# Kernel optimization log

Measured on AMD Instinct MI355X. Metric: run time of the kernel, lower is better.

## Reference

```python
import jax, jax.numpy as jnp
import numpy as np

NUM_NODES = 6144
INPUT_DIM = 128
OUTPUT_DIM = 128
NUM_HEADS = 4
HEAD_DIM = OUTPUT_DIM // NUM_HEADS
NEG_INF = -9e15  # mask constant used by the original module


def setup_inputs() -> dict:
    key = jax.random.key(0)
    k_x, k_adj, k_W, k_a = jax.random.split(key, 4)
    x = jax.random.normal(k_x, (NUM_NODES, INPUT_DIM), dtype=jnp.float32)
    adj = jax.random.randint(k_adj, (NUM_NODES, NUM_NODES), 0, 2, dtype=jnp.int32)
    # kaiming-uniform-ish init scale
    W = jax.random.uniform(k_W, (NUM_HEADS, INPUT_DIM, HEAD_DIM), dtype=jnp.float32,
                           minval=-1.0, maxval=1.0) * np.sqrt(6.0 / INPUT_DIM)
    a = jax.random.uniform(k_a, (NUM_HEADS, 2 * HEAD_DIM, 1), dtype=jnp.float32,
                           minval=-1.0, maxval=1.0) * np.sqrt(6.0 / (2 * HEAD_DIM))
    return {"x": x, "adj": adj, "W": W, "a": a}


def reference(x, adj, W, a):
    # x: [N, Din], adj: [N, N] int, W: [H, Din, d], a: [H, 2d, 1]
    H, Din, d = W.shape
    N = x.shape[0]
    h = jnp.einsum('ni,hid->hnd', x, W)               # [H, N, d] per-head projections
    a_dst = a[:, :d, 0]                                # applied to h_j (column / source of message)
    a_src = a[:, d:, 0]                                # applied to h_i (row / destination)
    s_dst = jnp.einsum('hnd,hd->hn', h, a_dst)         # [H, N]
    s_src = jnp.einsum('hnd,hd->hn', h, a_src)         # [H, N]
    # energy[h, i, j] = leaky_relu(a1 . h_j + a2 . h_i), same as concat-attention
    energy = jax.nn.leaky_relu(s_src[:, :, None] + s_dst[:, None, :], negative_slope=0.2)
    energy = jnp.where(adj[None] > 0, energy, NEG_INF)  # [H, N, N]
    attention = jax.nn.softmax(energy, axis=-1)
    h_prime = jnp.einsum('hij,hjd->hid', attention, h)  # [H, N, d]
    # faithful to torch h_prime.view(num_nodes, -1) on a contiguous [H,N,d] tensor
    return jnp.reshape(h_prime, (N, H * d))
```

## Files before the change

### kernel.cpp

```cpp
#include <hip/hip_runtime.h>
#include <stdint.h>

#define N_NODES 6144
#define LOG2E 1.44269504088896f

typedef float f32x4 __attribute__((ext_vector_type(4)));
typedef float f32x2 __attribute__((ext_vector_type(2)));
typedef short short8 __attribute__((ext_vector_type(8)));
typedef unsigned int uint32;
typedef unsigned long long uint64;

extern "C" __device__ float __ocml_native_exp2_f32(float);

__device__ __forceinline__ unsigned int pack2bf(float a, float b) {
  unsigned int ua = __float_as_uint(a) + 0x8000u;
  unsigned int ub = __float_as_uint(b) + 0x8000u;
  return __builtin_amdgcn_perm(ub, ua, 0x07060302u);
}

__device__ __forceinline__ uint32 bitmask32(uint32 bits, int j) {
#if __has_builtin(__builtin_amdgcn_sbfe)
  return (uint32)__builtin_amdgcn_sbfe((int)bits, (uint32)j, 1u);
#else
  return (uint32)(((int)(bits << (31 - j))) >> 31);
#endif
}

__global__ __launch_bounds__(256) void k0_pack(const int* __restrict__ adj,
                                               uint64* __restrict__ mask64) {
  int t = threadIdx.x;
  int wid = t >> 6, lane = t & 63;
  int row = blockIdx.x * 4 + wid;
  const int* ar = adj + (size_t)row * N_NODES + lane;
  uint64* mr = mask64 + (size_t)row * 96;
  #pragma unroll 8
  for (int c = 0; c < 96; ++c) {
    int v = ar[c << 6];
    uint64 b = __ballot(v != 0);
    if (lane == (c & 63)) mr[c] = b;
  }
}

__global__ __launch_bounds__(256) void k1_feat(const float* __restrict__ x,
                                               const float* __restrict__ W,
                                               const float* __restrict__ a,
                                               unsigned short* __restrict__ hfF,
                                               float* __restrict__ s_src2,
                                               float* __restrict__ s_dst2) {
  __shared__ float xl[64][132];
  __shared__ float Wl[64][128];
  int t = threadIdx.x;
  int n0 = blockIdx.x * 64;
  for (int u = t; u < 2048; u += 256) {
    int row = u >> 5, c4 = (u & 31) << 2;
    *(float4*)&xl[row][c4] = *(const float4*)(x + (size_t)(n0 + row) * 128 + c4);
  }
  int cg = t & 31, c0 = cg << 2;
  int ng = t >> 5, nb = ng << 3;
  float acc[8][4] = {};
  for (int ic = 0; ic < 2; ++ic) {
    __syncthreads();
    for (int u = t; u < 2048; u += 256) {
      int ii = u >> 5, c4 = (u & 31) << 2;
      int hh = c4 >> 5, d0 = c4 & 31;
      *(float4*)&Wl[ii][c4] = *(const float4*)(W + hh * 4096 + (ic * 64 + ii) * 32 + d0);
    }
    __syncthreads();
    #pragma unroll 4
    for (int ii = 0; ii < 64; ++ii) {
      float4 wv = *(float4*)&Wl[ii][c0];
      int i = ic * 64 + ii;
      #pragma unroll
      for (int r = 0; r < 8; ++r) {
        float xv = xl[nb + r][i];
        acc[r][0] += xv * wv.x; acc[r][1] += xv * wv.y;
        acc[r][2] += xv * wv.z; acc[r][3] += xv * wv.w;
      }
    }
  }
  __syncthreads();
  unsigned short* tb = (unsigned short*)&xl[0][0];
  float* pb = &Wl[0][0];
  int hh = c0 >> 5, d0 = c0 & 31;
  float4 adv = *(const float4*)(a + hh * 64 + d0);
  float4 asv = *(const float4*)(a + hh * 64 + 32 + d0);
  #pragma unroll
  for (int cc = 0; cc < 4; ++cc) {
    unsigned int* dst = (unsigned int*)(tb + (c0 + cc) * 66 + nb);
    #pragma unroll
    for (int p = 0; p < 4; ++p)
      dst[p] = pack2bf(acc[2 * p][cc], acc[2 * p + 1][cc]);
  }
  #pragma unroll
  for (int r = 0; r < 8; ++r) {
    float pd = acc[r][0] * adv.x + acc[r][1] * adv.y + acc[r][2] * adv.z + acc[r][3] * adv.w;
    float ps = acc[r][0] * asv.x + acc[r][1] * asv.y + acc[r][2] * asv.z + acc[r][3] * asv.w;
    pb[(nb + r) * 33 + cg] = pd;
    pb[2112 + (nb + r) * 33 + cg] = ps;
  }
  __syncthreads();
  {
    #pragma unroll
    for (int p = 0; p < 4; ++p) {
      int chunk = (p << 2) + (t >> 6);
      int lane = t & 63, mm = lane & 15, qq = lane >> 4;
      int h2 = chunk >> 2, kbl = (chunk >> 1) & 1, ff = chunk & 1;
      const unsigned int* s32 = (const unsigned int*)(
          tb + (h2 * 32 + ff * 16 + mm) * 66 + kbl * 32 + (qq << 3));
      int4 v;
      v.x = s32[0]; v.y = s32[1]; v.z = s32[2]; v.w = s32[3];
      int kbg = (n0 >> 5) + kbl;
      *(int4*)(hfF + (size_t)(((h2 * 192 + kbg) * 2 + ff) * 64 + lane) * 8) = v;
    }
  }
  for (int task = t; task < 512; task += 256) {
    int n = task & 63, hz = task >> 6;
    int h = hz & 3, sdx = hz >> 2;
    const float* src = pb + sdx * 2112 + n * 33 + h * 8;
    float s = src[0] + src[1] + src[2] + src[3] + src[4] + src[5] + src[6] + src[7];
    float* out = sdx ? s_src2 : s_dst2;
    out[h * N_NODES + n0 + n] = s * LOG2E;
  }
}

__device__ __forceinline__ void gat_tile(float ss, uint32 bits8,
                                         const f32x2 (&dv)[4], short8 b0, short8 b1,
                                         short8 ones, f32x4& a0, f32x4& a1, f32x4& az) {
  union { uint32 u4[4]; short8 v; } afr;
  f32x2 ss2;
  ss2[0] = ss; ss2[1] = ss;
  #pragma unroll
  for (int p = 0; p < 4; ++p) {
    f32x2 e = ss2 + dv[p];
    f32x2 e5 = e * 0.2f;
    float lrl = fmaxf(e[0], e5[0]);
    float lrh = fmaxf(e[1], e5[1]);
    float exl = __ocml_native_exp2_f32(lrl);
    float exh = __ocml_native_exp2_f32(lrh);
    uint32 wl = __float_as_uint(exl) & bitmask32(bits8, 2 * p);
    uint32 wh = __float_as_uint(exh) & bitmask32(bits8, 2 * p + 1);
    uint32 pk;
    asm("v_cvt_pk_bf16_f32 %0, %1, %2"
        : "=v"(pk)
        : "v"(__uint_as_float(wl)), "v"(__uint_as_float(wh)));
    afr.u4[p] = pk;
  }
  a0 = __builtin_amdgcn_mfma_f32_16x16x32_bf16(afr.v, b0, a0, 0, 0, 0);
  a1 = __builtin_amdgcn_mfma_f32_16x16x32_bf16(afr.v, b1, a1, 0, 0, 0);
  az = __builtin_amdgcn_mfma_f32_16x16x32_bf16(afr.v, ones, az, 0, 0, 0);
}

__device__ __forceinline__ void step2(uint32 w0, uint32 w1,
                                      int sh, const float* sdp, int koff,
                                      int4 B0i, int4 B1i, short8 ones,
                                      float ss0, float ss1,
                                      f32x4& a00, f32x4& a01, f32x4& a10, f32x4& a11,
                                      f32x4& az0, f32x4& az1) {
  union { f32x4 q[2]; f32x2 d[4]; } du;
  du.q[0] = *(const f32x4*)(sdp + koff);
  du.q[1] = *(const f32x4*)(sdp + koff + 4);
  union { int4 i; short8 v; } b0u, b1u;
  b0u.i = B0i; b1u.i = B1i;
  gat_tile(ss0, (w0 >> sh), du.d, b0u.v, b1u.v, ones, a00, a01, az0);
  gat_tile(ss1, (w1 >> sh), du.d, b0u.v, b1u.v, ones, a10, a11, az1);
}

__global__ __launch_bounds__(256, 4) void k2_attn(const uint32* __restrict__ maskw,
                                                  const unsigned short* __restrict__ hfF,
                                                  const float* __restrict__ s_src2,
                                                  const float* __restrict__ s_dst2,
                                                  float* __restrict__ Zpart,
                                                  float* __restrict__ part) {
  __shared__ float sd[4][768];
  __shared__ uint32 mlds[32 * 24];
  int t = threadIdx.x;
  int h = t >> 6, lane = t & 63, m = lane & 15, quad = lane >> 4;
  int sh = quad << 3;
  int bx = blockIdx.x;
  int slice = bx & 7, mg = bx >> 3;
  int i0 = mg << 5, kbase = slice * 768;
  {
    const float4* g = (const float4*)s_dst2;
    float4* l = (float4*)sd;
    int kb4 = kbase >> 2;
    #pragma unroll
    for (int r = 0; r < 3; ++r) {
      int u = t + (r << 8);
      int hx = u / 192, uu = u - hx * 192;
      l[hx * 192 + uu] = g[hx * 1536 + kb4 + uu];
    }
  }
  for (int r = t; r < 768; r += 256) {
    int row = r / 24, w = r - row * 24;
    mlds[r] = maskw[(size_t)(i0 + row) * 192 + slice * 24 + w];
  }
  float ss0 = s_src2[h * N_NODES + i0 + m];
  float ss1 = s_src2[h * N_NODES + i0 + 16 + m];
  __syncthreads();

  const unsigned short* hfb = hfF + (size_t)(h * 192 + slice * 24) * 1024 + lane * 8;
  const float* sdp = &sd[h][0] + sh;

  f32x4 a00 = {0,0,0,0}, a01 = {0,0,0,0};
  f32x4 a10 = {0,0,0,0}, a11 = {0,0,0,0};
  f32x4 az0 = {0,0,0,0}, az1 = {0,0,0,0};
  union { uint32 u[4]; short8 v; } ones;
  #pragma unroll
  for (int q = 0; q < 4; ++q) ones.u[q] = 0x3F803F80u;

  #pragma unroll 1
  for (int o = 0; o < 6; ++o) {
    const unsigned short* gb = hfb + o * 4096;
    int4 B00 = *(const int4*)(gb);
    int4 B01 = *(const int4*)(gb + 512);
    int4 B10 = *(const int4*)(gb + 1024);
    int4 B11 = *(const int4*)(gb + 1536);
    int4 B20 = *(const int4*)(gb + 2048);
    int4 B21 = *(const int4*)(gb + 2560);
    int4 B30 = *(const int4*)(gb + 3072);
    int4 B31 = *(const int4*)(gb + 3584);
    uint4 M0 = *(const uint4*)&mlds[m * 24 + (o << 2)];
    uint4 M1 = *(const uint4*)&mlds[(16 + m) * 24 + (o << 2)];
    __builtin_amdgcn_sched_barrier(0);
    int ko = o << 7;
    step2(M0.x, M1.x, sh, sdp, ko,      B00, B01, ones.v, ss0, ss1,
          a00, a01, a10, a11, az0, az1);
    step2(M0.y, M1.y, sh, sdp, ko + 32, B10, B11, ones.v, ss0, ss1,
          a00, a01, a10, a11, az0, az1);
    step2(M0.z, M1.z, sh, sdp, ko + 64, B20, B21, ones.v, ss0, ss1,
          a00, a01, a10, a11, az0, az1);
    step2(M0.w, M1.w, sh, sdp, ko + 96, B30, B31, ones.v, ss0, ss1,
          a00, a01, a10, a11, az0, az1);
  }

  if (m == 0) {
    float* zb = Zpart + (size_t)slice * 24576 + h * N_NODES + i0 + (quad << 2);
    #pragma unroll
    for (int r = 0; r < 4; ++r) {
      zb[r] = az0[r];
      zb[16 + r] = az1[r];
    }
  }
  float* pb = part + (size_t)slice * 786432 + (size_t)h * (N_NODES * 32) +
              (size_t)i0 * 32;
  #pragma unroll
  for (int r = 0; r < 4; ++r) {
    int row = (quad << 2) + r;
    pb[row * 32 + m] = a00[r];
    pb[row * 32 + 16 + m] = a01[r];
    pb[(16 + row) * 32 + m] = a10[r];
    pb[(16 + row) * 32 + 16 + m] = a11[r];
  }
}

__global__ __launch_bounds__(256) void k3_final(const float* __restrict__ part,
                                                const float* __restrict__ Zpart,
                                                float* __restrict__ out) {
  unsigned int idx4 = blockIdx.x * 256 + threadIdx.x;
  unsigned int h = idx4 / 49152u;
  unsigned int i = (idx4 - h * 49152u) >> 3;
  float z = 0.f;
  #pragma unroll
  for (int s = 0; s < 8; ++s) z += Zpart[s * 24576u + h * N_NODES + i];
  f32x4 p = {0.f, 0.f, 0.f, 0.f};
  const f32x4* P = (const f32x4*)part;
  #pragma unroll
  for (int s = 0; s < 8; ++s) p += P[(size_t)s * 196608u + idx4];
  float rz = 1.0f / z;
  ((f32x4*)out)[idx4] = p * rz;
}

extern "C" void kernel_launch(void* const* d_in, const int* in_sizes, int n_in,
                              void* d_out, int out_size, void* d_ws, size_t ws_size,
                              hipStream_t stream) {
  const float* x = (const float*)d_in[0];
  const int* adj = (const int*)d_in[1];
  const float* W = (const float*)d_in[2];
  const float* a = (const float*)d_in[3];
  float* out = (float*)d_out;

  float* wsf = (float*)d_ws;
  unsigned short* hfF = (unsigned short*)wsf;
  float* s_src2 = wsf + 393216;
  float* s_dst2 = s_src2 + 24576;
  float* part   = s_dst2 + 24576;
  float* Zpart  = part + 8 * 786432;
  uint64* mask64 = (uint64*)(Zpart + 8 * 24576);

  hipLaunchKernelGGL(k0_pack, dim3(1536), dim3(256), 0, stream, adj, mask64);
  hipLaunchKernelGGL(k1_feat, dim3(96), dim3(256), 0, stream, x, W, a, hfF, s_src2, s_dst2);
  hipLaunchKernelGGL(k2_attn, dim3(1536), dim3(256), 0, stream,
                     (const uint32*)mask64, hfF, s_src2, s_dst2, Zpart, part);
  hipLaunchKernelGGL(k3_final, dim3(768), dim3(256), 0, stream, part, Zpart, out);
}
```

Baseline: 305.8 us.

## Fuse adjacency bit-packing into attention kernel with double-buffered mask prefetch

Removes the separate pack kernel and its mask round trip through global memory. The attention kernel now reads the int32 adjacency directly, ballots it into bitmasks in double-buffered LDS, and prefetches the next chunk while the current one is computed. The K split per block goes from 8 slices to 4, with a larger s_dst tile, half the grid and fewer partials for the final reduction. The cost is a __syncthreads per iteration, more registers for the prefetched values, lower occupancy (launch bounds 3), and adjacency reads now sit inside the compute loop.

Result: faster. 255.1 us (-16.6%).

```diff
diff --git a/kernel.cpp b/kernel.cpp
--- a/kernel.cpp
+++ b/kernel.cpp
@@ -24,21 +24,6 @@
 #else
   return (uint32)(((int)(bits << (31 - j))) >> 31);
 #endif
-}
-
-__global__ __launch_bounds__(256) void k0_pack(const int* __restrict__ adj,
-                                               uint64* __restrict__ mask64) {
-  int t = threadIdx.x;
-  int wid = t >> 6, lane = t & 63;
-  int row = blockIdx.x * 4 + wid;
-  const int* ar = adj + (size_t)row * N_NODES + lane;
-  uint64* mr = mask64 + (size_t)row * 96;
-  #pragma unroll 8
-  for (int c = 0; c < 96; ++c) {
-    int v = ar[c << 6];
-    uint64 b = __ballot(v != 0);
-    if (lane == (c & 63)) mr[c] = b;
-  }
 }
 
 __global__ __launch_bounds__(256) void k1_feat(const float* __restrict__ x,
@@ -165,40 +150,46 @@
   gat_tile(ss1, (w1 >> sh), du.d, b0u.v, b1u.v, ones, a10, a11, az1);
 }
 
-__global__ __launch_bounds__(256, 4) void k2_attn(const uint32* __restrict__ maskw,
+__global__ __launch_bounds__(256, 3) void k2_attn(const int* __restrict__ adj,
                                                   const unsigned short* __restrict__ hfF,
                                                   const float* __restrict__ s_src2,
                                                   const float* __restrict__ s_dst2,
                                                   float* __restrict__ Zpart,
                                                   float* __restrict__ part) {
-  __shared__ float sd[4][768];
-  __shared__ uint32 mlds[32 * 24];
+  __shared__ float sd[4][1536];
+  __shared__ uint32 mlds[2][32][4];
   int t = threadIdx.x;
   int h = t >> 6, lane = t & 63, m = lane & 15, quad = lane >> 4;
   int sh = quad << 3;
   int bx = blockIdx.x;
-  int slice = bx & 7, mg = bx >> 3;
-  int i0 = mg << 5, kbase = slice * 768;
+  int slice = bx & 3, mg = bx >> 2;
+  int i0 = mg << 5, kbase = slice * 1536;
   {
     const float4* g = (const float4*)s_dst2;
     float4* l = (float4*)sd;
-    int kb4 = kbase >> 2;
-    #pragma unroll
-    for (int r = 0; r < 3; ++r) {
+    int kb4 = slice * 384;
+    #pragma unroll
+    for (int r = 0; r < 6; ++r) {
       int u = t + (r << 8);
-      int hx = u / 192, uu = u - hx * 192;
-      l[hx * 192 + uu] = g[hx * 1536 + kb4 + uu];
-    }
-  }
-  for (int r = t; r < 768; r += 256) {
-    int row = r / 24, w = r - row * 24;
-    mlds[r] = maskw[(size_t)(i0 + row) * 192 + slice * 24 + w];
+      int hx = u / 384, uu = u - hx * 384;
+      l[hx * 384 + uu] = g[hx * 1536 + kb4 + uu];
+    }
+  }
+  const int* arow = adj + (size_t)(i0 + (h << 3)) * N_NODES + kbase + lane;
+  {
+    #pragma unroll
+    for (int r = 0; r < 16; ++r) {
+      int v = arow[(r >> 1) * N_NODES + ((r & 1) << 6)];
+      uint64 b = __ballot(v != 0);
+      if (lane == r)
+        *(uint64*)&mlds[0][(h << 3) + (r >> 1)][(r & 1) << 1] = b;
+    }
   }
   float ss0 = s_src2[h * N_NODES + i0 + m];
   float ss1 = s_src2[h * N_NODES + i0 + 16 + m];
   __syncthreads();
 
-  const unsigned short* hfb = hfF + (size_t)(h * 192 + slice * 24) * 1024 + lane * 8;
+  const unsigned short* hfb = hfF + (size_t)(h * 192 + slice * 48) * 1024 + lane * 8;
   const float* sdp = &sd[h][0] + sh;
 
   f32x4 a00 = {0,0,0,0}, a01 = {0,0,0,0};
@@ -209,7 +200,8 @@
   for (int q = 0; q < 4; ++q) ones.u[q] = 0x3F803F80u;
 
   #pragma unroll 1
-  for (int o = 0; o < 6; ++o) {
+  for (int o = 0; o < 12; ++o) {
+    int cur = o & 1, nxt = cur ^ 1;
     const unsigned short* gb = hfb + o * 4096;
     int4 B00 = *(const int4*)(gb);
     int4 B01 = *(const int4*)(gb + 512);
@@ -219,8 +211,15 @@
     int4 B21 = *(const int4*)(gb + 2560);
     int4 B30 = *(const int4*)(gb + 3072);
     int4 B31 = *(const int4*)(gb + 3584);
-    uint4 M0 = *(const uint4*)&mlds[m * 24 + (o << 2)];
-    uint4 M1 = *(const uint4*)&mlds[(16 + m) * 24 + (o << 2)];
+    int pv[16];
+    if (o < 11) {
+      const int* ap = arow + ((o + 1) << 7);
+      #pragma unroll
+      for (int r = 0; r < 16; ++r)
+        pv[r] = ap[(r >> 1) * N_NODES + ((r & 1) << 6)];
+    }
+    uint4 M0 = *(const uint4*)&mlds[cur][m][0];
+    uint4 M1 = *(const uint4*)&mlds[cur][16 + m][0];
     __builtin_amdgcn_sched_barrier(0);
     int ko = o << 7;
     step2(M0.x, M1.x, sh, sdp, ko,      B00, B01, ones.v, ss0, ss1,
@@ -231,6 +230,16 @@
           a00, a01, a10, a11, az0, az1);
     step2(M0.w, M1.w, sh, sdp, ko + 96, B30, B31, ones.v, ss0, ss1,
           a00, a01, a10, a11, az0, az1);
+    __builtin_amdgcn_sched_barrier(0);
+    if (o < 11) {
+      #pragma unroll
+      for (int r = 0; r < 16; ++r) {
+        uint64 b = __ballot(pv[r] != 0);
+        if (lane == r)
+          *(uint64*)&mlds[nxt][(h << 3) + (r >> 1)][(r & 1) << 1] = b;
+      }
+    }
+    __syncthreads();
   }
 
   if (m == 0) {
@@ -261,11 +270,11 @@
   unsigned int i = (idx4 - h * 49152u) >> 3;
   float z = 0.f;
   #pragma unroll
-  for (int s = 0; s < 8; ++s) z += Zpart[s * 24576u + h * N_NODES + i];
+  for (int s = 0; s < 4; ++s) z += Zpart[s * 24576u + h * N_NODES + i];
   f32x4 p = {0.f, 0.f, 0.f, 0.f};
   const f32x4* P = (const f32x4*)part;
   #pragma unroll
-  for (int s = 0; s < 8; ++s) p += P[(size_t)s * 196608u + idx4];
+  for (int s = 0; s < 4; ++s) p += P[(size_t)s * 196608u + idx4];
   float rz = 1.0f / z;
   ((f32x4*)out)[idx4] = p * rz;
 }
@@ -284,12 +293,10 @@
   float* s_src2 = wsf + 393216;
   float* s_dst2 = s_src2 + 24576;
   float* part   = s_dst2 + 24576;
-  float* Zpart  = part + 8 * 786432;
-  uint64* mask64 = (uint64*)(Zpart + 8 * 24576);
-
-  hipLaunchKernelGGL(k0_pack, dim3(1536), dim3(256), 0, stream, adj, mask64);
+  float* Zpart  = part + 4 * 786432;
+
   hipLaunchKernelGGL(k1_feat, dim3(96), dim3(256), 0, stream, x, W, a, hfF, s_src2, s_dst2);
-  hipLaunchKernelGGL(k2_attn, dim3(1536), dim3(256), 0, stream,
-                     (const uint32*)mask64, hfF, s_src2, s_dst2, Zpart, part);
+  hipLaunchKernelGGL(k2_attn, dim3(768), dim3(256), 0, stream,
+                     adj, hfF, s_src2, s_dst2, Zpart, part);
   hipLaunchKernelGGL(k3_final, dim3(768), dim3(256), 0, stream, part, Zpart, out);
 }
```
